# Performance work log

Measured on AMD Instinct MI355X. Metric: run time of the kernel, lower is better.

The kernel has to match this reference:

```python
import jax, jax.numpy as jnp
import numpy as np

FEATURE_DIM = 68
ONE_HOT_MAX = 29  # one-hot coordinate features only for coords < 29


def _compute_encodings(height, width):
    # height, width are static Python ints
    xs = jnp.arange(width, dtype=jnp.float32)
    ys = jnp.arange(height, dtype=jnp.float32)

    def axis_feats(coords, size):
        if size > 1:
            norm = 2.0 * (coords / (size - 1)) - 1.0
            angle = jnp.pi * (coords / (size - 1))
        else:
            norm = jnp.zeros_like(coords)
            angle = jnp.zeros_like(coords)
        sign = jnp.sign(coords - size / 2.0)  # -1 / 0 / +1 around midpoint
        rtan = jnp.round(jnp.tan(angle))
        return jnp.stack([norm, sign, jnp.sin(angle), jnp.cos(angle), rtan], axis=-1)  # [size, 5]

    xf = axis_feats(xs, width)    # [W, 5] -> feature slots 0,2,4,6,8
    yf = axis_feats(ys, height)   # [H, 5] -> feature slots 1,3,5,7,9

    xb = jnp.broadcast_to(xf[None, :, :], (height, width, 5))
    yb = jnp.broadcast_to(yf[:, None, :], (height, width, 5))
    # interleave x/y features -> order x0,y0,x1,y1,... matches slots 0..9
    first10 = jnp.stack([xb, yb], axis=-1).reshape(height, width, 10)

    idx = jnp.arange(ONE_HOT_MAX)
    ohx = (xs[:, None] == idx[None, :]).astype(jnp.float32)  # [W, 29], zero rows for x >= 29
    ohy = (ys[:, None] == idx[None, :]).astype(jnp.float32)  # [H, 29]
    ohx_b = jnp.broadcast_to(ohx[None, :, :], (height, width, ONE_HOT_MAX))
    ohy_b = jnp.broadcast_to(ohy[:, None, :], (height, width, ONE_HOT_MAX))

    return jnp.concatenate([first10, ohx_b, ohy_b], axis=-1)  # [H, W, 68]


def setup_inputs() -> dict:
    key = jax.random.key(0)
    H, W, B = 512, 512, 8
    x = jax.random.normal(key, (B, H * W), dtype=jnp.float32)
    return {"x": x, "height": H, "width": W}


def reference(x, height, width):
    batch_size, seq_len = x.shape
    enc = _compute_encodings(height, width).reshape(-1, FEATURE_DIM)  # [H*W, 68]
    enc_b = jnp.broadcast_to(enc[None, :, :], (batch_size, seq_len, FEATURE_DIM))
    return jnp.concatenate([x[..., None], enc_b], axis=-1)  # [B, H*W, 69]
```

## Files before the change

### kernel.cpp

```cpp
#include <hip/hip_runtime.h>
#include <math.h>

typedef float f32x4 __attribute__((ext_vector_type(4)));

#define NF 69u
#define TROWS 64u
#define TILE_FLOATS (TROWS * NF)
#define TILE_F4 (TILE_FLOATS / 4u)
#define BLOCK 256u

__global__ void pe_table_kernel(const int* __restrict__ hptr,
                                const int* __restrict__ wptr,
                                float* __restrict__ tab8) {
    const int H = *hptr;
    const int W = *wptr;
    const int total = W + H;
    for (int i = (int)(blockIdx.x * blockDim.x + threadIdx.x); i < total;
         i += (int)(gridDim.x * blockDim.x)) {
        const bool is_y = (i >= W);
        const int c = is_y ? (i - W) : i;
        const int size = is_y ? H : W;
        double norm = 0.0, angle = 0.0;
        if (size > 1) {
            const double r = (double)c / (double)(size - 1);
            norm = 2.0 * r - 1.0;
            angle = M_PI * r;
        }
        const double d = (double)c - 0.5 * (double)size;
        const float sgn = (d > 0.0) ? 1.0f : ((d < 0.0) ? -1.0f : 0.0f);
        const int base = (is_y ? 8 * W : 0) + 8 * c;
        tab8[base + 0] = (float)norm;
        tab8[base + 1] = sgn;
        tab8[base + 2] = (float)sin(angle);
        tab8[base + 3] = (float)cos(angle);
        tab8[base + 4] = (float)rint(tan(angle));
    }
}

__device__ __forceinline__ void pe_compute(
    float* __restrict__ buf, unsigned int T, unsigned int Q,
    unsigned int W, unsigned int H, unsigned int yoff8,
    bool pot, unsigned int lw,
    const float* __restrict__ x, const float* __restrict__ tab8,
    unsigned int lane, unsigned int wv,
    unsigned int& pw, unsigned int& ph) {
    const unsigned int q = T * TROWS + lane;
    const bool valid = q < Q;
    unsigned int w, h;
    if (pot) {
        w = q & (W - 1u);
        h = (q >> lw) & (H - 1u);
    } else {
        const unsigned int t = q / W;
        w = q - t * W;
        h = t - (t / H) * H;
    }
    float* row = buf + lane * NF;
    const float* tx = tab8 + 8u * w;
    const float* ty = tab8 + yoff8 + 8u * h;
    if (wv == 0u) {
        if (valid) { row[0] = x[q]; row[1] = tx[0]; row[2] = ty[0]; }
    } else if (wv == 1u) {
        if (valid) { row[3] = tx[1]; row[4] = ty[1]; row[5] = tx[2]; }
    } else if (wv == 2u) {
        if (valid) { row[6] = ty[2]; row[7] = tx[3]; }
        if (pw < 29u) row[11u + pw] = 0.0f;
        const unsigned int npw = (valid && w < 29u) ? w : 0xFFFFFFFFu;
        if (npw < 29u) row[11u + npw] = 1.0f;
        pw = npw;
    } else {
        if (valid) { row[8] = ty[3]; row[9] = tx[4]; row[10] = ty[4]; }
        if (ph < 29u) row[40u + ph] = 0.0f;
        const unsigned int nph = (valid && h < 29u) ? h : 0xFFFFFFFFu;
        if (nph < 29u) row[40u + nph] = 1.0f;
        ph = nph;
    }
}

__global__ __launch_bounds__(BLOCK) void pe_main_kernel(
    const float* __restrict__ x,
    const int* __restrict__ hptr, const int* __restrict__ wptr,
    const float* __restrict__ tab8,
    float* __restrict__ out, unsigned int Q ) {
    __shared__ __align__(16) float lds[2][TILE_FLOATS];

    const unsigned int W = (unsigned int)*wptr;
    const unsigned int H = (unsigned int)*hptr;
    const unsigned int yoff8 = 8u * W;
    const bool pot = ((W & (W - 1u)) == 0u) && ((H & (H - 1u)) == 0u);
    const unsigned int lw = pot ? (unsigned int)(__ffs((int)W) - 1) : 0u;
    const unsigned int lane = threadIdx.x & 63u;
    const unsigned int wv = threadIdx.x >> 6;
    const unsigned int ntiles = (Q + TROWS - 1u) / TROWS;
    const unsigned int g = gridDim.x;

    {
        f32x4 z = {0.f, 0.f, 0.f, 0.f};
        f32x4* bp = (f32x4*)&lds[0][0];
        for (unsigned int j = threadIdx.x; j < 2u * TILE_F4; j += BLOCK)
            bp[j] = z;
    }
    __syncthreads();

    unsigned int T = blockIdx.x;
    if (T >= ntiles) return;

    unsigned int pw0 = 0xFFFFFFFFu, ph0 = 0xFFFFFFFFu;
    unsigned int pw1 = 0xFFFFFFFFu, ph1 = 0xFFFFFFFFu;
    pe_compute(lds[0], T, Q, W, H, yoff8, pot, lw, x, tab8, lane, wv, pw0, ph0);
    unsigned int cur = 0u;

    for (; T < ntiles; T += g) {
        asm volatile("s_waitcnt lgkmcnt(0)\n\ts_barrier" ::: "memory");

        const unsigned int rem = Q - T * TROWS;
        const size_t obase = (size_t)T * (size_t)TILE_FLOATS;
        const f32x4* lp = (const f32x4*)(cur ? lds[1] : lds[0]);
        f32x4* op = (f32x4*)(out + obase);

        if (rem >= TROWS) {
            const unsigned int t0 = threadIdx.x;
            const bool m = t0 < (TILE_F4 - 4u * BLOCK);
            f32x4 v0 = lp[t0];
            f32x4 v1 = lp[t0 + 256u];
            f32x4 v2 = lp[t0 + 512u];
            f32x4 v3 = lp[t0 + 768u];
            f32x4 v4;
            if (m) v4 = lp[t0 + 1024u];
            __builtin_nontemporal_store(v0, op + t0);
            __builtin_nontemporal_store(v1, op + t0 + 256u);
            __builtin_nontemporal_store(v2, op + t0 + 512u);
            __builtin_nontemporal_store(v3, op + t0 + 768u);
            if (m) __builtin_nontemporal_store(v4, op + t0 + 1024u);
        } else {
            const unsigned int nfl = rem * NF;
            const unsigned int n4 = nfl >> 2;
            const float* lf = (const float*)lp;
            for (unsigned int j = threadIdx.x; j < n4; j += BLOCK)
                __builtin_nontemporal_store(lp[j], op + j);
            for (unsigned int j = (n4 << 2) + threadIdx.x; j < nfl; j += BLOCK)
                __builtin_nontemporal_store(lf[j], out + obase + j);
        }

        const unsigned int Tn = T + g;
        if (Tn < ntiles) {
            if (cur == 0u)
                pe_compute(lds[1], Tn, Q, W, H, yoff8, pot, lw, x, tab8,
                           lane, wv, pw1, ph1);
            else
                pe_compute(lds[0], Tn, Q, W, H, yoff8, pot, lw, x, tab8,
                           lane, wv, pw0, ph0);
        }
        cur ^= 1u;
    }
}

extern "C" void kernel_launch(void* const* d_in, const int* in_sizes, int n_in,
                              void* d_out, int out_size, void* d_ws, size_t ws_size,
                              hipStream_t stream) {
    const float* x = (const float*)d_in[0];
    const int* hptr = (const int*)d_in[1];
    const int* wptr = (const int*)d_in[2];
    float* out = (float*)d_out;
    float* tab8 = (float*)d_ws;

    pe_table_kernel<<<8, 256, 0, stream>>>(hptr, wptr, tab8);

    const unsigned int Q = (unsigned int)in_sizes[0];
    const unsigned int ntiles = (Q + TROWS - 1u) / TROWS;
    unsigned int blocks = ntiles < 2048u ? ntiles : 2048u;
    if (blocks == 0u) blocks = 1u;
    pe_main_kernel<<<blocks, BLOCK, 0, stream>>>(x, hptr, wptr, tab8, out, Q);
}
```

Measured before the change: 119.7 us.

## Prefetch next tile's table and x loads before barrier; write full one-hot rows

The global loads of x and the per-coordinate table entries for the next tile are now issued into registers before the barrier, so their latency overlaps with storing the current tile. Wave 0 now loads all table values with vector loads and writes all 11 scalar features, and the four waves split the 58 one-hot columns between them. Every column is written explicitly, which replaces the previous incremental set/clear scheme and the initial LDS zero-fill. The cost is more LDS writes per row and more live registers, in a kernel that is mostly bound by output write bandwidth.

```diff
diff --git a/kernel.cpp b/kernel.cpp
--- a/kernel.cpp
+++ b/kernel.cpp
@@ -37,43 +37,68 @@
     }
 }
 
-__device__ __forceinline__ void pe_compute(
-    float* __restrict__ buf, unsigned int T, unsigned int Q,
-    unsigned int W, unsigned int H, unsigned int yoff8,
-    bool pot, unsigned int lw,
-    const float* __restrict__ x, const float* __restrict__ tab8,
+struct Regs {
+    unsigned int w, h;
+    bool valid;
+    f32x4 xa, ya;
+    float xa4, ya4, xv;
+};
+
+__device__ __forceinline__ void pe_load(
+    Regs& r, unsigned int T, unsigned int Q, unsigned int W, unsigned int H,
+    bool pot, unsigned int lw, unsigned int yoff8,
     unsigned int lane, unsigned int wv,
-    unsigned int& pw, unsigned int& ph) {
+    const float* __restrict__ x, const float* __restrict__ tab8) {
     const unsigned int q = T * TROWS + lane;
-    const bool valid = q < Q;
-    unsigned int w, h;
+    r.valid = q < Q;
     if (pot) {
-        w = q & (W - 1u);
-        h = (q >> lw) & (H - 1u);
+        r.w = q & (W - 1u);
+        r.h = (q >> lw) & (H - 1u);
     } else {
         const unsigned int t = q / W;
-        w = q - t * W;
-        h = t - (t / H) * H;
+        r.w = q - t * W;
+        r.h = t % H;
     }
+    if (wv == 0u && r.valid) {
+        r.xa  = *(const f32x4*)(tab8 + 8u * r.w);
+        r.xa4 = tab8[8u * r.w + 4u];
+        r.ya  = *(const f32x4*)(tab8 + yoff8 + 8u * r.h);
+        r.ya4 = tab8[yoff8 + 8u * r.h + 4u];
+        r.xv  = x[q];
+    }
+}
+
+__device__ __forceinline__ void pe_compute(float* __restrict__ buf,
+                                           const Regs& r,
+                                           unsigned int lane,
+                                           unsigned int wv) {
+    if (!r.valid) return;
     float* row = buf + lane * NF;
-    const float* tx = tab8 + 8u * w;
-    const float* ty = tab8 + yoff8 + 8u * h;
     if (wv == 0u) {
-        if (valid) { row[0] = x[q]; row[1] = tx[0]; row[2] = ty[0]; }
+        row[0] = r.xv;
+        row[1] = r.xa[0]; row[2]  = r.ya[0];
+        row[3] = r.xa[1]; row[4]  = r.ya[1];
+        row[5] = r.xa[2]; row[6]  = r.ya[2];
+        row[7] = r.xa[3]; row[8]  = r.ya[3];
+        row[9] = r.xa4;   row[10] = r.ya4;
+#pragma unroll
+        for (unsigned int f = 11u; f < 17u; ++f)
+            row[f] = (r.w == f - 11u) ? 1.0f : 0.0f;
     } else if (wv == 1u) {
-        if (valid) { row[3] = tx[1]; row[4] = ty[1]; row[5] = tx[2]; }
+#pragma unroll
+        for (unsigned int f = 17u; f < 34u; ++f)
+            row[f] = (r.w == f - 11u) ? 1.0f : 0.0f;
     } else if (wv == 2u) {
-        if (valid) { row[6] = ty[2]; row[7] = tx[3]; }
-        if (pw < 29u) row[11u + pw] = 0.0f;
-        const unsigned int npw = (valid && w < 29u) ? w : 0xFFFFFFFFu;
-        if (npw < 29u) row[11u + npw] = 1.0f;
-        pw = npw;
+#pragma unroll
+        for (unsigned int f = 34u; f < 40u; ++f)
+            row[f] = (r.w == f - 11u) ? 1.0f : 0.0f;
+#pragma unroll
+        for (unsigned int f = 40u; f < 51u; ++f)
+            row[f] = (r.h == f - 40u) ? 1.0f : 0.0f;
     } else {
-        if (valid) { row[8] = ty[3]; row[9] = tx[4]; row[10] = ty[4]; }
-        if (ph < 29u) row[40u + ph] = 0.0f;
-        const unsigned int nph = (valid && h < 29u) ? h : 0xFFFFFFFFu;
-        if (nph < 29u) row[40u + nph] = 1.0f;
-        ph = nph;
+#pragma unroll
+        for (unsigned int f = 51u; f < 69u; ++f)
+            row[f] = (r.h == f - 40u) ? 1.0f : 0.0f;
     }
 }
 
@@ -88,29 +113,27 @@
     const unsigned int H = (unsigned int)*hptr;
     const unsigned int yoff8 = 8u * W;
     const bool pot = ((W & (W - 1u)) == 0u) && ((H & (H - 1u)) == 0u);
-    const unsigned int lw = pot ? (unsigned int)(__ffs((int)W) - 1) : 0u;
+    const unsigned int lw = pot ? (unsigned int)(31 - __clz((int)W)) : 0u;
     const unsigned int lane = threadIdx.x & 63u;
     const unsigned int wv = threadIdx.x >> 6;
     const unsigned int ntiles = (Q + TROWS - 1u) / TROWS;
     const unsigned int g = gridDim.x;
 
-    {
-        f32x4 z = {0.f, 0.f, 0.f, 0.f};
-        f32x4* bp = (f32x4*)&lds[0][0];
-        for (unsigned int j = threadIdx.x; j < 2u * TILE_F4; j += BLOCK)
-            bp[j] = z;
-    }
-    __syncthreads();
-
     unsigned int T = blockIdx.x;
     if (T >= ntiles) return;
 
-    unsigned int pw0 = 0xFFFFFFFFu, ph0 = 0xFFFFFFFFu;
-    unsigned int pw1 = 0xFFFFFFFFu, ph1 = 0xFFFFFFFFu;
-    pe_compute(lds[0], T, Q, W, H, yoff8, pot, lw, x, tab8, lane, wv, pw0, ph0);
+    Regs rr;
+    pe_load(rr, T, Q, W, H, pot, lw, yoff8, lane, wv, x, tab8);
+    pe_compute(lds[0], rr, lane, wv);
     unsigned int cur = 0u;
 
     for (; T < ntiles; T += g) {
+        const unsigned int Tn = T + g;
+
+        Regs rn;
+        if (Tn < ntiles)
+            pe_load(rn, Tn, Q, W, H, pot, lw, yoff8, lane, wv, x, tab8);
+
         asm volatile("s_waitcnt lgkmcnt(0)\n\ts_barrier" ::: "memory");
 
         const unsigned int rem = Q - T * TROWS;
@@ -120,18 +143,18 @@
 
         if (rem >= TROWS) {
             const unsigned int t0 = threadIdx.x;
-            const bool m = t0 < (TILE_F4 - 4u * BLOCK);
             f32x4 v0 = lp[t0];
+            __builtin_nontemporal_store(v0, op + t0);
             f32x4 v1 = lp[t0 + 256u];
+            __builtin_nontemporal_store(v1, op + t0 + 256u);
             f32x4 v2 = lp[t0 + 512u];
+            __builtin_nontemporal_store(v2, op + t0 + 512u);
             f32x4 v3 = lp[t0 + 768u];
-            f32x4 v4;
-            if (m) v4 = lp[t0 + 1024u];
-            __builtin_nontemporal_store(v0, op + t0);
-            __builtin_nontemporal_store(v1, op + t0 + 256u);
-            __builtin_nontemporal_store(v2, op + t0 + 512u);
             __builtin_nontemporal_store(v3, op + t0 + 768u);
-            if (m) __builtin_nontemporal_store(v4, op + t0 + 1024u);
+            if (t0 < TILE_F4 - 1024u) {
+                f32x4 v4 = lp[t0 + 1024u];
+                __builtin_nontemporal_store(v4, op + t0 + 1024u);
+            }
         } else {
             const unsigned int nfl = rem * NF;
             const unsigned int n4 = nfl >> 2;
@@ -142,15 +165,8 @@
                 __builtin_nontemporal_store(lf[j], out + obase + j);
         }
 
-        const unsigned int Tn = T + g;
-        if (Tn < ntiles) {
-            if (cur == 0u)
-                pe_compute(lds[1], Tn, Q, W, H, yoff8, pot, lw, x, tab8,
-                           lane, wv, pw1, ph1);
-            else
-                pe_compute(lds[0], Tn, Q, W, H, yoff8, pot, lw, x, tab8,
-                           lane, wv, pw0, ph0);
-        }
+        if (Tn < ntiles)
+            pe_compute(cur ? lds[0] : lds[1], rn, lane, wv);
         cur ^= 1u;
     }
 }
```

After: 119.0 us. No clear change (-0.6%).
